# Kernel tuning notes

Measured on AMD Instinct MI355X. Metric: run time of the kernel, lower is better.

Reference implementation:

```python
import jax, jax.numpy as jnp
import numpy as np

B, N, F_IN, F_OUT, E, GSD = 64, 512, 512, 512, 4, 1024
EPS = 1e-5


def _bn(z2d, gamma, beta):
    # training-mode BatchNorm1d over rows, biased variance, eps=1e-5
    mean = z2d.mean(axis=0)
    var = z2d.var(axis=0)
    return (z2d - mean) * jax.lax.rsqrt(var + EPS) * gamma + beta


def setup_inputs() -> dict:
    key = jax.random.key(0)
    ks = jax.random.split(key, 10)
    x = jax.random.normal(ks[0], (B, N, F_IN), dtype=jnp.float32)
    adj = jax.random.uniform(ks[1], (B, E, N, N), dtype=jnp.float32)
    global_state = jax.random.normal(ks[2], (B, GSD), dtype=jnp.float32)
    subgraph_sizes = jax.random.randint(ks[3], (B, 2), 0, 256, dtype=jnp.int64)
    mask = jnp.ones((B, N, 1), dtype=jnp.float32)
    # parameters
    W_gfc = jax.random.normal(ks[4], (GSD // 2, F_OUT), dtype=jnp.float32) * (1.0 / np.sqrt(GSD // 2))
    b_gfc = jnp.zeros((F_OUT,), dtype=jnp.float32)
    W_gc = jax.random.normal(ks[5], (E, F_IN + F_OUT, F_OUT), dtype=jnp.float32) * (1.0 / np.sqrt(F_IN + F_OUT))
    b_gc = jnp.zeros((F_OUT,), dtype=jnp.float32)
    gamma_n = jnp.ones((F_OUT,), dtype=jnp.float32)
    beta_n = jnp.zeros((F_OUT,), dtype=jnp.float32)
    gamma_g = jnp.ones((F_OUT,), dtype=jnp.float32)
    beta_g = jnp.zeros((F_OUT,), dtype=jnp.float32)
    return dict(x=x, adj=adj, global_state=global_state, subgraph_sizes=subgraph_sizes,
                mask=mask, W_gfc=W_gfc, b_gfc=b_gfc, W_gc=W_gc, b_gc=b_gc,
                gamma_n=gamma_n, beta_n=beta_n, gamma_g=gamma_g, beta_g=beta_g)


def reference(x, adj, global_state, subgraph_sizes, mask,
              W_gfc, b_gfc, W_gc, b_gc, gamma_n, beta_n, gamma_g, beta_g):
    b, n, _ = x.shape
    o = W_gfc.shape[1]
    # global FC on the two halves of the global state
    gs = global_state.reshape(b, 2, -1)                 # [B,2,GSD/2]
    gt = jnp.einsum('bkg,go->bko', gs, W_gfc) + b_gfc   # [B,2,O]
    # data-dependent broadcast of global features into node slices (vectorized)
    n1 = subgraph_sizes[:, 0]
    n2 = subgraph_sizes[:, 1]
    idx = jnp.arange(n)[None, :]
    sel0 = (idx < n1[:, None]).astype(x.dtype)                                  # [B,N]
    sel1 = ((idx >= n1[:, None]) & (idx < (n1 + n2)[:, None])).astype(x.dtype)  # [B,N]
    bg = sel0[..., None] * gt[:, 0, None, :] + sel1[..., None] * gt[:, 1, None, :]  # [B,N,O]
    x_concat = jnp.concatenate([x, bg], axis=-1)        # [B,N,F_IN+O]
    # multi-relational graph convolution: sum_e adj_e @ (x W_e) + bias
    support = jnp.einsum('bnf,efo->beno', x_concat, W_gc)       # [B,E,N,O]
    x_out = jnp.einsum('benm,bemo->bno', adj, support) + b_gc   # [B,N,O]
    # BN + mask + relu on nodes
    x_out = _bn(x_out.reshape(-1, o), gamma_n, beta_n).reshape(b, n, o)
    x_out = jax.nn.relu(x_out * mask)
    # BN + relu on global
    g_out = _bn(gt.reshape(-1, o), gamma_g, beta_g).reshape(b, 2, o)
    g_out = jax.nn.relu(g_out).reshape(b, -1)
    return x_out, g_out
```

## Files before the change

kernel.cpp:

```cpp
#include <hip/hip_runtime.h>

#define DEVI __device__ __forceinline__

typedef __bf16 bf16x8 __attribute__((ext_vector_type(8)));
typedef float  f32x4  __attribute__((ext_vector_type(4)));
typedef unsigned short ushort8_t __attribute__((ext_vector_type(8)));

constexpr size_t XOUT_ELEMS = (size_t)64 * 512 * 512;

DEVI unsigned short f2b(float f) {
  __bf16 h = (__bf16)f;
  return __builtin_bit_cast(unsigned short, h);
}

__global__ void k_decode(const int* __restrict__ ss, int* __restrict__ ns) {
  int t = threadIdx.x;
  int odd = ss[2 * t + 1];
  unsigned long long bal = __ballot(odd == 0);
  bool is64 = (bal == 0xFFFFFFFFFFFFFFFFull);
  if (is64) {
    const long long* s64 = (const long long*)ss;
    ns[2 * t]     = (int)s64[2 * t];
    ns[2 * t + 1] = (int)s64[2 * t + 1];
  } else {
    ns[2 * t]     = ss[2 * t];
    ns[2 * t + 1] = ss[2 * t + 1];
  }
}

__global__ void k_gt(const float* __restrict__ gs, const float* __restrict__ W,
                     const float* __restrict__ bias, float* __restrict__ gt,
                     unsigned short* __restrict__ gth) {
  __shared__ float srow[4][512];
  int r0  = blockIdx.y * 4;
  int col = blockIdx.x * 256 + threadIdx.x;
  for (int i = threadIdx.x; i < 4 * 512; i += 256)
    srow[i >> 9][i & 511] = gs[(size_t)r0 * 512 + i];
  __syncthreads();
  float acc[4] = {0.f, 0.f, 0.f, 0.f};
  for (int g = 0; g < 512; ++g) {
    float w = W[(size_t)g * 512 + col];
    acc[0] += srow[0][g] * w;
    acc[1] += srow[1][g] * w;
    acc[2] += srow[2][g] * w;
    acc[3] += srow[3][g] * w;
  }
  float bb = bias[col];
  #pragma unroll
  for (int r = 0; r < 4; ++r) {
    float v = acc[r] + bb;
    gt [(size_t)(r0 + r) * 512 + col] = v;
    gth[(size_t)(r0 + r) * 512 + col] = f2b(v);
  }
}

__global__ void k_gbn(const float* __restrict__ gt, const float* __restrict__ gamma,
                      const float* __restrict__ beta, float* __restrict__ gout) {
  int col = blockIdx.x * 64 + threadIdx.x;
  float s = 0.f, q = 0.f;
  for (int r = 0; r < 128; ++r) {
    float v = gt[(size_t)r * 512 + col];
    s += v; q += v * v;
  }
  float m   = s * (1.f / 128.f);
  float var = q * (1.f / 128.f) - m * m;
  float inv = 1.f / sqrtf(var + 1e-5f);
  float g = gamma[col], b = beta[col];
  for (int r = 0; r < 128; ++r) {
    float v = (gt[(size_t)r * 512 + col] - m) * inv * g + b;
    gout[(size_t)r * 512 + col] = fmaxf(v, 0.f);
  }
}

__global__ void k_cvt(const float* __restrict__ in, unsigned short* __restrict__ out,
                      long n8) {
  long i = (long)blockIdx.x * blockDim.x + threadIdx.x;
  long stride = (long)gridDim.x * blockDim.x;
  for (; i < n8; i += stride) {
    float4 a = ((const float4*)in)[2 * i];
    float4 b = ((const float4*)in)[2 * i + 1];
    ushort8_t o;
    o[0] = f2b(a.x); o[1] = f2b(a.y); o[2] = f2b(a.z); o[3] = f2b(a.w);
    o[4] = f2b(b.x); o[5] = f2b(b.y); o[6] = f2b(b.z); o[7] = f2b(b.w);
    *(ushort8_t*)&out[i * 8] = o;
  }
}

__global__ void k_cvt_w(const float* __restrict__ W, unsigned short* __restrict__ wT) {
  __shared__ float t[32][33];
  int k0 = blockIdx.x * 32, o0 = blockIdx.y * 32, e = blockIdx.z;
  const float* Wb = W + (size_t)e * 1024 * 512;
  unsigned short* Tb = wT + (size_t)e * 512 * 1024;
  int tid = threadIdx.x;
  #pragma unroll
  for (int p = 0; p < 4; ++p) {
    int kl = p * 8 + (tid >> 5), ol = tid & 31;
    t[kl][ol] = Wb[(size_t)(k0 + kl) * 512 + o0 + ol];
  }
  __syncthreads();
  #pragma unroll
  for (int p = 0; p < 4; ++p) {
    int ol = p * 8 + (tid >> 5), kl = tid & 31;
    Tb[(size_t)(o0 + ol) * 1024 + k0 + kl] = f2b(t[kl][ol]);
  }
}

DEVI void gl_lds16(const unsigned short* g, unsigned short* l) {
  __builtin_amdgcn_global_load_lds(
      (const __attribute__((address_space(1))) void*)g,
      (__attribute__((address_space(3))) void*)l, 16, 0, 0);
}

DEVI int lds_idx(int row, int slot) {
  return row * 32 + ((slot ^ ((row >> 1) & 3)) << 3);
}

template <class FA, class FB>
DEVI void mfma_core(unsigned short* As, unsigned short* Bs, FA srcA, FB srcB,
                    int NT, f32x4 (&acc)[4][4]) {
  const int tid  = threadIdx.x;
  const int lane = tid & 63;
  const int wave = tid >> 6;
  const int wr = wave >> 1, wc = wave & 1;
  const int fr = lane & 15, fs = lane >> 4;

  const int c0 = tid,      r0 = c0 >> 2, s0 = (c0 & 3) ^ ((r0 >> 1) & 3);
  const int c1 = tid + 256, r1 = c1 >> 2, s1 = (c1 & 3) ^ ((r1 >> 1) & 3);

  int aoff[4], boff[4];
  #pragma unroll
  for (int i = 0; i < 4; ++i) {
    aoff[i] = lds_idx(wr * 64 + i * 16 + fr, fs);
    boff[i] = lds_idx(wc * 64 + i * 16 + fr, fs);
  }

  gl_lds16(srcA(r0, s0 * 8, 0), As + c0 * 8);
  gl_lds16(srcA(r1, s1 * 8, 0), As + c1 * 8);
  gl_lds16(srcB(r0, s0 * 8, 0), Bs + c0 * 8);
  gl_lds16(srcB(r1, s1 * 8, 0), Bs + c1 * 8);

  for (int kt = 0; kt < NT; ++kt) {
    __syncthreads();
    bf16x8 af[4], bf[4];
    #pragma unroll
    for (int i = 0; i < 4; ++i) af[i] = *(const bf16x8*)(As + aoff[i]);
    #pragma unroll
    for (int j = 0; j < 4; ++j) bf[j] = *(const bf16x8*)(Bs + boff[j]);
    if (kt + 1 < NT) {
      __syncthreads();
      gl_lds16(srcA(r0, s0 * 8, kt + 1), As + c0 * 8);
      gl_lds16(srcA(r1, s1 * 8, kt + 1), As + c1 * 8);
      gl_lds16(srcB(r0, s0 * 8, kt + 1), Bs + c0 * 8);
      gl_lds16(srcB(r1, s1 * 8, kt + 1), Bs + c1 * 8);
    }
    #pragma unroll
    for (int i = 0; i < 4; ++i)
      #pragma unroll
      for (int j = 0; j < 4; ++j)
        acc[i][j] = __builtin_amdgcn_mfma_f32_16x16x32_bf16(af[i], bf[j], acc[i][j], 0, 0, 0);
  }
}

__global__ __launch_bounds__(256) void k_support(
    const unsigned short* __restrict__ xh, const unsigned short* __restrict__ gth,
    const unsigned short* __restrict__ wT, const int* __restrict__ ns,
    const unsigned short* __restrict__ zb, unsigned short* __restrict__ supT, int b0) {
  __shared__ __align__(16) unsigned short As[4096], Bs[4096];
  const int otile = blockIdx.x * 128;
  const int row0  = blockIdx.y * 128;
  const int e  = blockIdx.z & 3;
  const int gi = blockIdx.z >> 2;
  const int b  = b0 + gi;
  const int n1  = ns[2 * b];
  const int n12 = n1 + ns[2 * b + 1];
  const unsigned short* xb = xh + (size_t)b * 512 * 512;
  const unsigned short* g0 = gth + (size_t)(2 * b) * 512;
  const unsigned short* g1 = g0 + 512;
  const unsigned short* wb = wT + (size_t)e * 512 * 1024;

  auto srcA = [=](int row, int kofs, int kt) -> const unsigned short* {
    int k  = kt * 32 + kofs;
    int rg = row0 + row;
    if (k < 512) return xb + (size_t)rg * 512 + k;
    int kk = k - 512;
    if (rg < n1)  return g0 + kk;
    if (rg < n12) return g1 + kk;
    return zb;
  };
  auto srcB = [=](int row, int kofs, int kt) -> const unsigned short* {
    return wb + (size_t)(otile + row) * 1024 + kt * 32 + kofs;
  };

  f32x4 acc[4][4];
  #pragma unroll
  for (int i = 0; i < 4; ++i)
    #pragma unroll
    for (int j = 0; j < 4; ++j) acc[i][j] = (f32x4){0.f, 0.f, 0.f, 0.f};

  mfma_core(As, Bs, srcA, srcB, 32, acc);

  const int lane = threadIdx.x & 63, wave = threadIdx.x >> 6;
  const int wr = wave >> 1, wc = wave & 1, fr = lane & 15, fs = lane >> 4;
  unsigned short* sp = supT + (size_t)(gi * 4 + e) * 262144;
  #pragma unroll
  for (int i = 0; i < 4; ++i) {
    int m = row0 + wr * 64 + i * 16 + fs * 4;
    #pragma unroll
    for (int j = 0; j < 4; ++j) {
      int o = otile + wc * 64 + j * 16 + fr;
      f32x4 v = acc[i][j];
      ushort4 h;
      h.x = f2b(v[0]); h.y = f2b(v[1]); h.z = f2b(v[2]); h.w = f2b(v[3]);
      *(ushort4*)&sp[(size_t)o * 512 + m] = h;
    }
  }
}

__global__ __launch_bounds__(256) void k_xout(
    const unsigned short* __restrict__ adjh, const unsigned short* __restrict__ supT,
    const float* __restrict__ bgc, float* __restrict__ out,
    float* __restrict__ gsum, float* __restrict__ gsq, int b0) {
  __shared__ __align__(16) unsigned short As[4096], Bs[4096];
  const int otile = blockIdx.x * 128;
  const int row0  = blockIdx.y * 128;
  const int gi = blockIdx.z;
  const int b  = b0 + gi;
  const unsigned short* ab = adjh + (size_t)b * 4 * 262144;
  const unsigned short* sb = supT + (size_t)gi * 4 * 262144;

  auto srcA = [=](int row, int kofs, int kt) -> const unsigned short* {
    int k = kt * 32 + kofs;
    int e = k >> 9, m = k & 511;
    return ab + ((size_t)e * 512 + row0 + row) * 512 + m;
  };
  auto srcB = [=](int row, int kofs, int kt) -> const unsigned short* {
    int k = kt * 32 + kofs;
    int e = k >> 9, m = k & 511;
    return sb + ((size_t)e * 512 + otile + row) * 512 + m;
  };

  f32x4 acc[4][4];
  #pragma unroll
  for (int i = 0; i < 4; ++i)
    #pragma unroll
    for (int j = 0; j < 4; ++j) acc[i][j] = (f32x4){0.f, 0.f, 0.f, 0.f};

  mfma_core(As, Bs, srcA, srcB, 64, acc);

  const int tid = threadIdx.x;
  const int lane = tid & 63, wave = tid >> 6;
  const int wr = wave >> 1, wc = wave & 1, fr = lane & 15, fs = lane >> 4;

  float cs[4], cq[4];
  #pragma unroll
  for (int j = 0; j < 4; ++j) {
    int o = otile + wc * 64 + j * 16 + fr;
    float bb = bgc[o];
    float s = 0.f, q = 0.f;
    #pragma unroll
    for (int i = 0; i < 4; ++i) {
      int nb = row0 + wr * 64 + i * 16 + fs * 4;
      #pragma unroll
      for (int r = 0; r < 4; ++r) {
        float v = acc[i][j][r] + bb;
        out[((size_t)b * 512 + nb + r) * 512 + o] = v;
        s += v; q += v * v;
      }
    }
    cs[j] = s; cq[j] = q;
  }

  __syncthreads();
  float* red = (float*)As;
  red[tid] = 0.f;
  __syncthreads();
  #pragma unroll
  for (int j = 0; j < 4; ++j) {
    int cl = wc * 64 + j * 16 + fr;
    atomicAdd(&red[cl], cs[j]);
    atomicAdd(&red[128 + cl], cq[j]);
  }
  __syncthreads();
  if (tid < 128) {
    atomicAdd(&gsum[otile + tid], red[tid]);
    atomicAdd(&gsq[otile + tid],  red[128 + tid]);
  }
}

__global__ void k_norm(const float* __restrict__ gsum, const float* __restrict__ gsq,
                       const float* __restrict__ gamma, const float* __restrict__ beta,
                       const float* __restrict__ mask, float* __restrict__ out) {
  __shared__ float sc[512], sh[512];
  for (int c = threadIdx.x; c < 512; c += blockDim.x) {
    float m   = gsum[c] * (1.f / 32768.f);
    float var = gsq[c] * (1.f / 32768.f) - m * m;
    float inv = 1.f / sqrtf(var + 1e-5f);
    float g = gamma[c] * inv;
    sc[c] = g;
    sh[c] = beta[c] - m * g;
  }
  __syncthreads();
  size_t i0 = (size_t)blockIdx.x * blockDim.x + threadIdx.x;
  size_t stride = (size_t)gridDim.x * blockDim.x;
  size_t n4 = XOUT_ELEMS / 4;
  for (size_t i = i0; i < n4; i += stride) {
    float4 p = ((const float4*)out)[i];
    int c = (int)((i * 4) & 511);
    size_t row = (i * 4) >> 9;
    float mk = mask[row];
    p.x = fmaxf((p.x * sc[c + 0] + sh[c + 0]) * mk, 0.f);
    p.y = fmaxf((p.y * sc[c + 1] + sh[c + 1]) * mk, 0.f);
    p.z = fmaxf((p.z * sc[c + 2] + sh[c + 2]) * mk, 0.f);
    p.w = fmaxf((p.w * sc[c + 3] + sh[c + 3]) * mk, 0.f);
    ((float4*)out)[i] = p;
  }
}

extern "C" void kernel_launch(void* const* d_in, const int* in_sizes, int n_in,
                              void* d_out, int out_size, void* d_ws, size_t ws_size,
                              hipStream_t stream) {
  const float* x    = (const float*)d_in[0];
  const float* adj  = (const float*)d_in[1];
  const float* gs   = (const float*)d_in[2];
  const int*   ssz  = (const int*)d_in[3];
  const float* mask = (const float*)d_in[4];
  const float* Wgfc = (const float*)d_in[5];
  const float* bgfc = (const float*)d_in[6];
  const float* Wgc  = (const float*)d_in[7];
  const float* bgc  = (const float*)d_in[8];
  const float* gn   = (const float*)d_in[9];
  const float* btn  = (const float*)d_in[10];
  const float* gg   = (const float*)d_in[11];
  const float* btg  = (const float*)d_in[12];
  float* out = (float*)d_out;

  char* w = (char*)d_ws;
  float*          gt   = (float*)w;
  unsigned short* gth  = (unsigned short*)(w + 262144);
  int*            ns   = (int*)(w + 393216);
  float*          gsum = (float*)(w + 393728);
  float*          gsq  = (float*)(w + 395776);
  unsigned short* zb   = (unsigned short*)(w + 397824);
  unsigned short* xh   = (unsigned short*)(w + ((size_t)1  << 20));
  unsigned short* wT   = (unsigned short*)(w + ((size_t)33 << 20));
  unsigned short* adjh = (unsigned short*)(w + ((size_t)37 << 20));
  unsigned short* supT = (unsigned short*)(w + ((size_t)165 << 20));

  long long avail = (long long)ws_size - (165ll << 20);
  int G = (avail > 0) ? (int)(avail / (2ll << 20)) : 0;
  if (G < 1) G = 1;
  if (G > 64) G = 64;

  k_decode<<<1, 64, 0, stream>>>(ssz, ns);
  k_gt<<<dim3(2, 32), 256, 0, stream>>>(gs, Wgfc, bgfc, gt, gth);
  k_gbn<<<8, 64, 0, stream>>>(gt, gg, btg, out + XOUT_ELEMS);
  hipMemsetAsync(gsum, 0, 5120, stream);

  k_cvt<<<2048, 256, 0, stream>>>(x, xh, (long)(16777216 / 8));
  k_cvt<<<4096, 256, 0, stream>>>(adj, adjh, (long)(67108864 / 8));
  k_cvt_w<<<dim3(32, 16, 4), 256, 0, stream>>>(Wgc, wT);

  for (int b0 = 0; b0 < 64; b0 += G) {
    int gc = 64 - b0; if (gc > G) gc = G;
    k_support<<<dim3(4, 4, 4 * gc), 256, 0, stream>>>(xh, gth, wT, ns, zb, supT, b0);
    k_xout<<<dim3(4, 4, gc), 256, 0, stream>>>(adjh, supT, bgc, out, gsum, gsq, b0);
  }

  k_norm<<<2048, 256, 0, stream>>>(gsum, gsq, gn, btn, mask, out);
}
```

Before: 830.8 us.

## Precompute global-feature projection and halve support GEMM K dimension

The global-feature half of the concatenated input is constant per segment, so its product with W_gc is precomputed once per batch-half by a small GEMM kernel (k_gadd). The support GEMM then only runs over the 512 x features and adds the precomputed row vector in the epilogue based on subgraph membership. This halves the support GEMM's K loop. Grids are also flattened so the batch index varies fastest, and the batch chunk size is capped at 16 instead of 64, which changes L2 locality and the supT working-set size. The precomputed term is added in fp32 before the bf16 rounding rather than being multiplied in bf16, which slightly changes rounding.

```diff
diff --git a/kernel.cpp b/kernel.cpp
--- a/kernel.cpp
+++ b/kernel.cpp
@@ -124,7 +124,7 @@
   const int wr = wave >> 1, wc = wave & 1;
   const int fr = lane & 15, fs = lane >> 4;
 
-  const int c0 = tid,      r0 = c0 >> 2, s0 = (c0 & 3) ^ ((r0 >> 1) & 3);
+  const int c0 = tid,       r0 = c0 >> 2, s0 = (c0 & 3) ^ ((r0 >> 1) & 3);
   const int c1 = tid + 256, r1 = c1 >> 2, s1 = (c1 & 3) ^ ((r1 >> 1) & 3);
 
   int aoff[4], boff[4];
@@ -161,31 +161,62 @@
   }
 }
 
-__global__ __launch_bounds__(256) void k_support(
-    const unsigned short* __restrict__ xh, const unsigned short* __restrict__ gth,
-    const unsigned short* __restrict__ wT, const int* __restrict__ ns,
-    const unsigned short* __restrict__ zb, unsigned short* __restrict__ supT, int b0) {
+__global__ __launch_bounds__(256) void k_gadd(
+    const unsigned short* __restrict__ gth, const unsigned short* __restrict__ wT,
+    float* __restrict__ gadd) {
   __shared__ __align__(16) unsigned short As[4096], Bs[4096];
   const int otile = blockIdx.x * 128;
-  const int row0  = blockIdx.y * 128;
-  const int e  = blockIdx.z & 3;
-  const int gi = blockIdx.z >> 2;
-  const int b  = b0 + gi;
+
+  auto srcA = [=](int row, int kofs, int kt) -> const unsigned short* {
+    return gth + (size_t)row * 512 + kt * 32 + kofs;
+  };
+  auto srcB = [=](int row, int kofs, int kt) -> const unsigned short* {
+    int op = otile + row;
+    int e = op >> 9, o = op & 511;
+    return wT + (size_t)e * 524288 + (size_t)o * 1024 + 512 + kt * 32 + kofs;
+  };
+
+  f32x4 acc[4][4];
+  #pragma unroll
+  for (int i = 0; i < 4; ++i)
+    #pragma unroll
+    for (int j = 0; j < 4; ++j) acc[i][j] = (f32x4){0.f, 0.f, 0.f, 0.f};
+
+  mfma_core(As, Bs, srcA, srcB, 16, acc);
+
+  const int lane = threadIdx.x & 63, wave = threadIdx.x >> 6;
+  const int wr = wave >> 1, wc = wave & 1, fr = lane & 15, fs = lane >> 4;
+  #pragma unroll
+  for (int i = 0; i < 4; ++i) {
+    int m = wr * 64 + i * 16 + fs * 4;
+    #pragma unroll
+    for (int j = 0; j < 4; ++j) {
+      int op = otile + wc * 64 + j * 16 + fr;
+      #pragma unroll
+      for (int r = 0; r < 4; ++r)
+        gadd[(size_t)(m + r) * 2048 + op] = acc[i][j][r];
+    }
+  }
+}
+
+__global__ __launch_bounds__(256) void k_support(
+    const unsigned short* __restrict__ xh, const unsigned short* __restrict__ wT,
+    const float* __restrict__ gadd, const int* __restrict__ ns,
+    unsigned short* __restrict__ supT, int b0, int gc) {
+  __shared__ __align__(16) unsigned short As[4096], Bs[4096];
+  int flat = blockIdx.x;
+  const int zi = flat % gc; flat /= gc;
+  const int e  = flat & 3;  flat >>= 2;
+  const int otile = (flat & 3) * 128;
+  const int row0  = (flat >> 2) * 128;
+  const int b  = b0 + zi;
   const int n1  = ns[2 * b];
   const int n12 = n1 + ns[2 * b + 1];
-  const unsigned short* xb = xh + (size_t)b * 512 * 512;
-  const unsigned short* g0 = gth + (size_t)(2 * b) * 512;
-  const unsigned short* g1 = g0 + 512;
-  const unsigned short* wb = wT + (size_t)e * 512 * 1024;
+  const unsigned short* xb = xh + (size_t)b * 262144;
+  const unsigned short* wb = wT + (size_t)e * 524288;
 
   auto srcA = [=](int row, int kofs, int kt) -> const unsigned short* {
-    int k  = kt * 32 + kofs;
-    int rg = row0 + row;
-    if (k < 512) return xb + (size_t)rg * 512 + k;
-    int kk = k - 512;
-    if (rg < n1)  return g0 + kk;
-    if (rg < n12) return g1 + kk;
-    return zb;
+    return xb + (size_t)(row0 + row) * 512 + kt * 32 + kofs;
   };
   auto srcB = [=](int row, int kofs, int kt) -> const unsigned short* {
     return wb + (size_t)(otile + row) * 1024 + kt * 32 + kofs;
@@ -197,20 +228,26 @@
     #pragma unroll
     for (int j = 0; j < 4; ++j) acc[i][j] = (f32x4){0.f, 0.f, 0.f, 0.f};
 
-  mfma_core(As, Bs, srcA, srcB, 32, acc);
+  mfma_core(As, Bs, srcA, srcB, 16, acc);
 
   const int lane = threadIdx.x & 63, wave = threadIdx.x >> 6;
   const int wr = wave >> 1, wc = wave & 1, fr = lane & 15, fs = lane >> 4;
-  unsigned short* sp = supT + (size_t)(gi * 4 + e) * 262144;
-  #pragma unroll
-  for (int i = 0; i < 4; ++i) {
-    int m = row0 + wr * 64 + i * 16 + fs * 4;
-    #pragma unroll
-    for (int j = 0; j < 4; ++j) {
-      int o = otile + wc * 64 + j * 16 + fr;
-      f32x4 v = acc[i][j];
+  unsigned short* sp = supT + (size_t)(zi * 4 + e) * 262144;
+  #pragma unroll
+  for (int j = 0; j < 4; ++j) {
+    int o = otile + wc * 64 + j * 16 + fr;
+    float g0 = gadd[(size_t)(2 * b)     * 2048 + e * 512 + o];
+    float g1 = gadd[(size_t)(2 * b + 1) * 2048 + e * 512 + o];
+    #pragma unroll
+    for (int i = 0; i < 4; ++i) {
+      int m = row0 + wr * 64 + i * 16 + fs * 4;
       ushort4 h;
-      h.x = f2b(v[0]); h.y = f2b(v[1]); h.z = f2b(v[2]); h.w = f2b(v[3]);
+      #pragma unroll
+      for (int r = 0; r < 4; ++r) {
+        int mr = m + r;
+        float add = (mr < n1) ? g0 : ((mr < n12) ? g1 : 0.f);
+        ((unsigned short*)&h)[r] = f2b(acc[i][j][r] + add);
+      }
       *(ushort4*)&sp[(size_t)o * 512 + m] = h;
     }
   }
@@ -219,14 +256,15 @@
 __global__ __launch_bounds__(256) void k_xout(
     const unsigned short* __restrict__ adjh, const unsigned short* __restrict__ supT,
     const float* __restrict__ bgc, float* __restrict__ out,
-    float* __restrict__ gsum, float* __restrict__ gsq, int b0) {
+    float* __restrict__ gsum, float* __restrict__ gsq, int b0, int gc) {
   __shared__ __align__(16) unsigned short As[4096], Bs[4096];
-  const int otile = blockIdx.x * 128;
-  const int row0  = blockIdx.y * 128;
-  const int gi = blockIdx.z;
-  const int b  = b0 + gi;
+  int flat = blockIdx.x;
+  const int zi = flat % gc; flat /= gc;
+  const int otile = (flat & 3) * 128;
+  const int row0  = (flat >> 2) * 128;
+  const int b  = b0 + zi;
   const unsigned short* ab = adjh + (size_t)b * 4 * 262144;
-  const unsigned short* sb = supT + (size_t)gi * 4 * 262144;
+  const unsigned short* sb = supT + (size_t)zi * 4 * 262144;
 
   auto srcA = [=](int row, int kofs, int kt) -> const unsigned short* {
     int k = kt * 32 + kofs;
@@ -337,33 +375,34 @@
   char* w = (char*)d_ws;
   float*          gt   = (float*)w;
   unsigned short* gth  = (unsigned short*)(w + 262144);
-  int*            ns   = (int*)(w + 393216);
-  float*          gsum = (float*)(w + 393728);
-  float*          gsq  = (float*)(w + 395776);
-  unsigned short* zb   = (unsigned short*)(w + 397824);
-  unsigned short* xh   = (unsigned short*)(w + ((size_t)1  << 20));
-  unsigned short* wT   = (unsigned short*)(w + ((size_t)33 << 20));
-  unsigned short* adjh = (unsigned short*)(w + ((size_t)37 << 20));
-  unsigned short* supT = (unsigned short*)(w + ((size_t)165 << 20));
-
-  long long avail = (long long)ws_size - (165ll << 20);
+  float*          gadd = (float*)(w + 393216);
+  int*            ns   = (int*)(w + 1441792);
+  float*          gsum = (float*)(w + 1442304);
+  float*          gsq  = (float*)(w + 1444352);
+  unsigned short* xh   = (unsigned short*)(w + ((size_t)2  << 20));
+  unsigned short* wT   = (unsigned short*)(w + ((size_t)34 << 20));
+  unsigned short* adjh = (unsigned short*)(w + ((size_t)40 << 20));
+  unsigned short* supT = (unsigned short*)(w + ((size_t)168 << 20));
+
+  long long avail = (long long)ws_size - (168ll << 20);
   int G = (avail > 0) ? (int)(avail / (2ll << 20)) : 0;
   if (G < 1) G = 1;
-  if (G > 64) G = 64;
+  if (G > 16) G = 16;
 
   k_decode<<<1, 64, 0, stream>>>(ssz, ns);
   k_gt<<<dim3(2, 32), 256, 0, stream>>>(gs, Wgfc, bgfc, gt, gth);
   k_gbn<<<8, 64, 0, stream>>>(gt, gg, btg, out + XOUT_ELEMS);
-  hipMemsetAsync(gsum, 0, 5120, stream);
+  hipMemsetAsync(gsum, 0, 4096, stream);
 
   k_cvt<<<2048, 256, 0, stream>>>(x, xh, (long)(16777216 / 8));
   k_cvt<<<4096, 256, 0, stream>>>(adj, adjh, (long)(67108864 / 8));
   k_cvt_w<<<dim3(32, 16, 4), 256, 0, stream>>>(Wgc, wT);
+  k_gadd<<<16, 256, 0, stream>>>(gth, wT, gadd);
 
   for (int b0 = 0; b0 < 64; b0 += G) {
     int gc = 64 - b0; if (gc > G) gc = G;
-    k_support<<<dim3(4, 4, 4 * gc), 256, 0, stream>>>(xh, gth, wT, ns, zb, supT, b0);
-    k_xout<<<dim3(4, 4, gc), 256, 0, stream>>>(adjh, supT, bgc, out, gsum, gsq, b0);
+    k_support<<<16 * 4 * gc, 256, 0, stream>>>(xh, wT, gadd, ns, supT, b0, gc);
+    k_xout<<<16 * gc, 256, 0, stream>>>(adjh, supT, bgc, out, gsum, gsq, b0, gc);
   }
 
   k_norm<<<2048, 256, 0, stream>>>(gsum, gsq, gn, btn, mask, out);
```

Result: slower. 893.0 us (+7.5%).
